# Performance work log

Measured on AMD Instinct MI355X. Metric: run time of the kernel, lower is better.

## Reference

```python
import jax, jax.numpy as jnp
import numpy as np

D_MODEL = 1024
NUM_HEADS = 16
D_K = D_MODEL // NUM_HEADS


def setup_inputs() -> dict:
    key = jax.random.key(0)
    ks = jax.random.split(key, 9)
    s = 1.0 / np.sqrt(D_MODEL)
    x = jax.random.normal(ks[0], (1, 4096, D_MODEL), dtype=jnp.float32)
    Wq = jax.random.uniform(ks[1], (D_MODEL, D_MODEL), jnp.float32, -s, s)
    bq = jax.random.uniform(ks[2], (D_MODEL,), jnp.float32, -s, s)
    Wk = jax.random.uniform(ks[3], (D_MODEL, D_MODEL), jnp.float32, -s, s)
    bk = jax.random.uniform(ks[4], (D_MODEL,), jnp.float32, -s, s)
    Wv = jax.random.uniform(ks[5], (D_MODEL, D_MODEL), jnp.float32, -s, s)
    bv = jax.random.uniform(ks[6], (D_MODEL,), jnp.float32, -s, s)
    Wo = jax.random.uniform(ks[7], (D_MODEL, D_MODEL), jnp.float32, -s, s)
    bo = jax.random.uniform(ks[8], (D_MODEL,), jnp.float32, -s, s)
    return {"x": x, "Wq": Wq, "bq": bq, "Wk": Wk, "bk": bk,
            "Wv": Wv, "bv": bv, "Wo": Wo, "bo": bo}


def reference(x, Wq, bq, Wk, bk, Wv, bv, Wo, bo):
    B, S, _ = x.shape
    scale = jnp.sqrt(jnp.asarray(D_K, dtype=x.dtype))
    # projections (torch Linear: y = x @ W.T + b)
    q = (x @ Wq.T + bq).reshape(B, S, NUM_HEADS, D_K).transpose(0, 2, 1, 3)
    k = (x @ Wk.T + bk).reshape(B, S, NUM_HEADS, D_K).transpose(0, 2, 1, 3)
    v = (x @ Wv.T + bv).reshape(B, S, NUM_HEADS, D_K).transpose(0, 2, 1, 3)
    # [B, H, S, S] naive scores, causal mask, softmax
    scores = jnp.einsum('bhqd,bhkd->bhqk', q, k) / scale
    causal = jnp.tril(jnp.ones((S, S), dtype=bool))
    scores = jnp.where(causal, scores, jnp.asarray(-jnp.inf, dtype=scores.dtype))
    probs = jax.nn.softmax(scores, axis=-1)
    out = jnp.einsum('bhqk,bhkd->bhqd', probs, v)
    out = out.transpose(0, 2, 1, 3).reshape(B, S, D_MODEL)
    return out @ Wo.T + bo
```

## Files before the change

### kernel.cpp

```cpp
#include <hip/hip_runtime.h>
#include <math.h>

#define SEQ 4096
#define DMODEL 1024
#define NH 16
#define DK 64
#define LDP 72

typedef __bf16    bf16x8 __attribute__((ext_vector_type(8)));
typedef float     f32x4  __attribute__((ext_vector_type(4)));
typedef __fp16    fp16x2 __attribute__((ext_vector_type(2)));
typedef _Float16  h16x2  __attribute__((ext_vector_type(2)));
typedef _Float16  h16x4  __attribute__((ext_vector_type(4)));
typedef _Float16  h16x8  __attribute__((ext_vector_type(8)));

#define GLOAD_LDS16(g, l) __builtin_amdgcn_global_load_lds(                     \
    (const __attribute__((address_space(1))) unsigned int*)(g),                 \
    (__attribute__((address_space(3))) unsigned int*)(l), 16, 0, 0)

__device__ __forceinline__ h16x2 cvt_pk_h16(float a, float b) {
    fp16x2 r = __builtin_amdgcn_cvt_pkrtz(a, b);
    return __builtin_bit_cast(h16x2, r);
}

#define EXP2R(x) __builtin_amdgcn_exp2f(x)

__global__ __launch_bounds__(256)
void cvt_all(const float* __restrict__ x, const float* __restrict__ Wq,
             const float* __restrict__ Wk, const float* __restrict__ Wv,
             const float* __restrict__ Wo, __bf16* __restrict__ dst)
{
    const size_t M1 = 1u << 20;
    const size_t e = ((size_t)blockIdx.x * 256 + threadIdx.x) * 8;
    const float* src; size_t off;
    if      (e < 4*M1) { src = x;  off = e;        }
    else if (e < 5*M1) { src = Wq; off = e - 4*M1; }
    else if (e < 6*M1) { src = Wk; off = e - 5*M1; }
    else if (e < 7*M1) { src = Wv; off = e - 6*M1; }
    else               { src = Wo; off = e - 7*M1; }
    const float4 f0 = *reinterpret_cast<const float4*>(&src[off]);
    const float4 f1 = *reinterpret_cast<const float4*>(&src[off + 4]);
    bf16x8 pk;
    pk[0]=(__bf16)f0.x; pk[1]=(__bf16)f0.y; pk[2]=(__bf16)f0.z; pk[3]=(__bf16)f0.w;
    pk[4]=(__bf16)f1.x; pk[5]=(__bf16)f1.y; pk[6]=(__bf16)f1.z; pk[7]=(__bf16)f1.w;
    *reinterpret_cast<bf16x8*>(&dst[e]) = pk;
}

__device__ __forceinline__ void gemm_core128(const __bf16* __restrict__ A,
                                             const __bf16* __restrict__ W,
                                             int m0, int n0, int t,
                                             __bf16* AsF, __bf16* BsF,
                                             f32x4 acc[4][4])
{
    const int w = t >> 6, lane = t & 63, l15 = lane & 15, quad = lane >> 4;
    const int wm = (w & 1) * 64, wn = (w >> 1) * 64;
    const int lr = lane >> 3, lc = lane & 7;
    for (int k0 = 0; k0 < DMODEL; k0 += 64) {
        __syncthreads();
        #pragma unroll
        for (int p = 0; p < 4; ++p) {
            const int n = w*4 + p;
            const int r = n*8 + lr;
            const int cl = lc ^ (r & 7);
            GLOAD_LDS16(&A[(size_t)(m0 + r) * DMODEL + k0 + cl*8], &AsF[n*512]);
            GLOAD_LDS16(&W[(size_t)(n0 + r) * DMODEL + k0 + cl*8], &BsF[n*512]);
        }
        __syncthreads();
        #pragma unroll
        for (int kb = 0; kb < 2; ++kb) {
            const int phys = ((kb*4 + quad) ^ (l15 & 7)) * 8;
            bf16x8 af[4], bfr[4];
            #pragma unroll
            for (int i = 0; i < 4; ++i) {
                af[i]  = *reinterpret_cast<const bf16x8*>(&AsF[(wm + i*16 + l15)*64 + phys]);
                bfr[i] = *reinterpret_cast<const bf16x8*>(&BsF[(wn + i*16 + l15)*64 + phys]);
            }
            #pragma unroll
            for (int ms = 0; ms < 4; ++ms)
                #pragma unroll
                for (int ns = 0; ns < 4; ++ns)
                    acc[ms][ns] = __builtin_amdgcn_mfma_f32_16x16x32_bf16(af[ms], bfr[ns], acc[ms][ns], 0, 0, 0);
        }
    }
}

__global__ __launch_bounds__(256, 3)
void gemm_qkv(const __bf16* __restrict__ xb, const __bf16* __restrict__ Wcat,
              const float* __restrict__ bq, const float* __restrict__ bk,
              const float* __restrict__ bv,
              _Float16* __restrict__ Qh, _Float16* __restrict__ Kh, _Float16* __restrict__ Vth)
{
    __shared__ __bf16 SM[4*64*LDP];
    __bf16* AsF = SM;
    __bf16* BsF = SM + 8192;
    const int t = threadIdx.x;
    const int n0g = blockIdx.x * 128;
    const int m0  = blockIdx.y * 128;
    const int which = n0g >> 10;
    const int n_in  = n0g & 1023;

    f32x4 acc[4][4] = {};
    gemm_core128(xb, Wcat, m0, n0g, t, AsF, BsF, acc);

    const int w = t >> 6, lane = t & 63, l15 = lane & 15, quad = lane >> 4;
    const int wm = (w & 1) * 64, wn = (w >> 1) * 64;
    const float* bias = (which == 0) ? bq : (which == 1) ? bk : bv;
    float br[4];
    #pragma unroll
    for (int ns = 0; ns < 4; ++ns) br[ns] = bias[n_in + wn + ns*16 + l15];

    if (which == 2) {
        #pragma unroll
        for (int ms = 0; ms < 4; ++ms)
            #pragma unroll
            for (int ns = 0; ns < 4; ++ns) {
                h16x4 pk;
                #pragma unroll
                for (int rg = 0; rg < 4; ++rg) pk[rg] = (_Float16)(acc[ms][ns][rg] + br[ns]);
                *reinterpret_cast<h16x4*>(
                    &Vth[(size_t)(n_in + wn + ns*16 + l15) * SEQ + m0 + wm + ms*16 + quad*4]) = pk;
            }
    } else {
        const float s = (which == 0) ? 0.1803368787f : 1.0f;
        _Float16* C = (which == 0) ? Qh : Kh;
        __syncthreads();
        _Float16* tile = (_Float16*)SM + w * 64 * LDP;
        #pragma unroll
        for (int ms = 0; ms < 4; ++ms)
            #pragma unroll
            for (int ns = 0; ns < 4; ++ns)
                #pragma unroll
                for (int rg = 0; rg < 4; ++rg)
                    tile[(ms*16 + quad*4 + rg) * LDP + ns*16 + l15] =
                        (_Float16)((acc[ms][ns][rg] + br[ns]) * s);
        asm volatile("s_waitcnt lgkmcnt(0)" ::: "memory");
        const int er = lane >> 3, ec = (lane & 7) * 8;
        #pragma unroll
        for (int p = 0; p < 8; ++p) {
            const h16x8 v = *reinterpret_cast<const h16x8*>(&tile[(er + p*8) * LDP + ec]);
            *reinterpret_cast<h16x8*>(
                &C[(size_t)(m0 + wm + er + p*8) * DMODEL + n_in + wn + ec]) = v;
        }
    }
}

__device__ __forceinline__ void gemm_core64(const __bf16* __restrict__ A,
                                            const __bf16* __restrict__ W,
                                            int m0, int n0, int t,
                                            __bf16* AsF, __bf16* BsF,
                                            f32x4 acc[2][4])
{
    const int w = t >> 6, lane = t & 63, l15 = lane & 15, quad = lane >> 4;
    const int lr = lane >> 3, lc = lane & 7;
    for (int k0 = 0; k0 < DMODEL; k0 += 64) {
        __syncthreads();
        #pragma unroll
        for (int p = 0; p < 4; ++p) {
            const int n = w*4 + p;
            const int r = n*8 + lr;
            const int cl = lc ^ (r & 7);
            GLOAD_LDS16(&A[(size_t)(m0 + r) * DMODEL + k0 + cl*8], &AsF[n*512]);
        }
        #pragma unroll
        for (int p = 0; p < 2; ++p) {
            const int n = w*2 + p;
            const int r = n*8 + lr;
            const int cl = lc ^ (r & 7);
            GLOAD_LDS16(&W[(size_t)(n0 + r) * DMODEL + k0 + cl*8], &BsF[n*512]);
        }
        __syncthreads();
        #pragma unroll
        for (int kb = 0; kb < 2; ++kb) {
            const int phys = ((kb*4 + quad) ^ (l15 & 7)) * 8;
            bf16x8 af0 = *reinterpret_cast<const bf16x8*>(&AsF[(w*32 + l15)*64 + phys]);
            bf16x8 af1 = *reinterpret_cast<const bf16x8*>(&AsF[(w*32 + 16 + l15)*64 + phys]);
            #pragma unroll
            for (int ns = 0; ns < 4; ++ns) {
                const bf16x8 bfr = *reinterpret_cast<const bf16x8*>(&BsF[(ns*16 + l15)*64 + phys]);
                acc[0][ns] = __builtin_amdgcn_mfma_f32_16x16x32_bf16(af0, bfr, acc[0][ns], 0, 0, 0);
                acc[1][ns] = __builtin_amdgcn_mfma_f32_16x16x32_bf16(af1, bfr, acc[1][ns], 0, 0, 0);
            }
        }
    }
}

__global__ __launch_bounds__(256, 4)
void gemm_out(const __bf16* __restrict__ Ob, const __bf16* __restrict__ Wob,
              const float* __restrict__ bo, float* __restrict__ out)
{
    __shared__ __bf16 AsF[128*64];
    __shared__ __bf16 BsF[64*64];
    const int t = threadIdx.x;
    const int n0 = blockIdx.x * 64;
    const int m0 = blockIdx.y * 128;

    f32x4 acc[2][4] = {};
    gemm_core64(Ob, Wob, m0, n0, t, AsF, BsF, acc);

    const int lane = t & 63, l15 = lane & 15, quad = lane >> 4, w = t >> 6;
    float br[4];
    #pragma unroll
    for (int ns = 0; ns < 4; ++ns) br[ns] = bo[n0 + ns*16 + l15];
    #pragma unroll
    for (int ms = 0; ms < 2; ++ms)
        #pragma unroll
        for (int ns = 0; ns < 4; ++ns)
            #pragma unroll
            for (int rg = 0; rg < 4; ++rg)
                out[(size_t)(m0 + w*32 + ms*16 + quad*4 + rg) * DMODEL + n0 + ns*16 + l15] =
                    acc[ms][ns][rg] + br[ns];
}

__global__ __launch_bounds__(256, 3)
void attn_mfma(const _Float16* __restrict__ Q, const _Float16* __restrict__ K,
               const _Float16* __restrict__ Vt, __bf16* __restrict__ O,
               _Float16* __restrict__ partA, _Float16* __restrict__ partB,
               float* __restrict__ lpart)
{
    __shared__ _Float16 KsF[2][64*64];
    __shared__ _Float16 VsF[2][64*64];

    const int t = threadIdx.x;
    const int w = t >> 6;
    const int lane = t & 63, l15 = lane & 15, quad = lane >> 4;
    const int lr = lane >> 3, lc = lane & 7;
    const int h = blockIdx.y;
    const int u = blockIdx.x;

    const int cl = lc ^ lr;
    const int rA = (w*2 + 0)*8 + lr, rB = (w*2 + 1)*8 + lr;
    const int dA = (w*2 + 0)*512,   dB = (w*2 + 1)*512;
    const h16x4 vone = {(_Float16)1.f, (_Float16)1.f, (_Float16)1.f, (_Float16)1.f};

    int g = u * 22;
    const int gend = g + 22;
    int qt = 0;
    while ((qt + 1) * (qt + 2) <= g) ++qt;

    while (g < gend) {
        const int S = qt * (qt + 1);
        const int rowlen = 2*qt + 2;
        const int ts = g - S;
        const int rem = gend - S;
        const int te = (rowlen < rem) ? rowlen : rem;
        const int s0 = qt*128 + w*16;
        const int s1 = s0 + 64;

        h16x8 bq8[2][2];
        #pragma unroll
        for (int kb = 0; kb < 2; ++kb) {
            bq8[0][kb] = *reinterpret_cast<const h16x8*>(
                &Q[(size_t)(s0 + l15) * DMODEL + h*DK + kb*32 + quad*8]);
            bq8[1][kb] = *reinterpret_cast<const h16x8*>(
                &Q[(size_t)(s1 + l15) * DMODEL + h*DK + kb*32 + quad*8]);
        }

        const _Float16* kpA = &K [(size_t)(ts*64 + rA) * DMODEL + h*DK + cl*8];
        const _Float16* kpB = &K [(size_t)(ts*64 + rB) * DMODEL + h*DK + cl*8];
        const _Float16* vpA = &Vt[(size_t)(h*DK + rA) * SEQ + ts*64 + cl*8];
        const _Float16* vpB = &Vt[(size_t)(h*DK + rB) * SEQ + ts*64 + cl*8];

#define STAGE_KV(bi) do {                                     \
        GLOAD_LDS16(kpA, &KsF[bi][dA]);                       \
        GLOAD_LDS16(kpB, &KsF[bi][dB]);                       \
        GLOAD_LDS16(vpA, &VsF[bi][dA]);                       \
        GLOAD_LDS16(vpB, &VsF[bi][dB]);                       \
        kpA += (size_t)64*DMODEL; kpB += (size_t)64*DMODEL;   \
        vpA += 64; vpB += 64; } while (0)

        f32x4 acc[2][4] = {};
        f32x4 accl[2] = {};

        STAGE_KV(0);
        __syncthreads();

        int pbuf = 0;
        for (int tk = ts; tk < te; ++tk, pbuf ^= 1) {
            if (tk + 1 < te) STAGE_KV(pbuf ^ 1);

            const int j0 = tk * 64;
            const bool act0 = (j0 <= s0 + 15);
            const bool msk0 = (j0 + 63 > s0);
            const bool msk1 = (j0 + 63 > s1);
            const int rel0 = s0 - j0 + l15;
            const int rel1 = s1 - j0 + l15;

            h16x4 ap[2][4];
            #pragma unroll
            for (int st = 0; st < 4; ++st) {
                const h16x8 ak0 = *reinterpret_cast<const h16x8*>(
                    &KsF[pbuf][(st*16 + l15)*64 + ((quad ^ (l15 & 7)))*8]);
                const h16x8 ak1 = *reinterpret_cast<const h16x8*>(
                    &KsF[pbuf][(st*16 + l15)*64 + (((4 + quad) ^ (l15 & 7)))*8]);
                {
                    f32x4 cc = {0.f, 0.f, 0.f, 0.f};
                    cc = __builtin_amdgcn_mfma_f32_16x16x32_f16(ak0, bq8[1][0], cc, 0, 0, 0);
                    cc = __builtin_amdgcn_mfma_f32_16x16x32_f16(ak1, bq8[1][1], cc, 0, 0, 0);
                    float pv[4];
                    if (msk1) {
                        #pragma unroll
                        for (int rg = 0; rg < 4; ++rg) {
                            const float e = EXP2R(cc[rg]);
                            pv[rg] = (st*16 + quad*4 + rg > rel1) ? 0.f : e;
                        }
                    } else {
                        #pragma unroll
                        for (int rg = 0; rg < 4; ++rg) pv[rg] = EXP2R(cc[rg]);
                    }
                    const h16x2 lo = cvt_pk_h16(pv[0], pv[1]);
                    const h16x2 hi = cvt_pk_h16(pv[2], pv[3]);
                    ap[1][st] = (h16x4){lo[0], lo[1], hi[0], hi[1]};
                    accl[1] = __builtin_amdgcn_mfma_f32_16x16x16f16(ap[1][st], vone, accl[1], 0, 0, 0);
                }
                if (act0) {
                    f32x4 cc = {0.f, 0.f, 0.f, 0.f};
                    cc = __builtin_amdgcn_mfma_f32_16x16x32_f16(ak0, bq8[0][0], cc, 0, 0, 0);
                    cc = __builtin_amdgcn_mfma_f32_16x16x32_f16(ak1, bq8[0][1], cc, 0, 0, 0);
                    float pv[4];
                    if (msk0) {
                        #pragma unroll
                        for (int rg = 0; rg < 4; ++rg) {
                            const float e = EXP2R(cc[rg]);
                            pv[rg] = (st*16 + quad*4 + rg > rel0) ? 0.f : e;
                        }
                    } else {
                        #pragma unroll
                        for (int rg = 0; rg < 4; ++rg) pv[rg] = EXP2R(cc[rg]);
                    }
                    const h16x2 lo = cvt_pk_h16(pv[0], pv[1]);
                    const h16x2 hi = cvt_pk_h16(pv[2], pv[3]);
                    ap[0][st] = (h16x4){lo[0], lo[1], hi[0], hi[1]};
                    accl[0] = __builtin_amdgcn_mfma_f32_16x16x16f16(ap[0][st], vone, accl[0], 0, 0, 0);
                }
            }

            #pragma unroll
            for (int ds_ = 0; ds_ < 4; ++ds_) {
                #pragma unroll
                for (int st = 0; st < 4; ++st) {
                    const h16x4 bv = *reinterpret_cast<const h16x4*>(
                        &VsF[pbuf][(ds_*16 + l15)*64 +
                                   (((st*2 + (quad >> 1)) ^ (l15 & 7)))*8 + (quad & 1)*4]);
                    acc[1][ds_] = __builtin_amdgcn_mfma_f32_16x16x16f16(ap[1][st], bv, acc[1][ds_], 0, 0, 0);
                    if (act0)
                        acc[0][ds_] = __builtin_amdgcn_mfma_f32_16x16x16f16(ap[0][st], bv, acc[0][ds_], 0, 0, 0);
                }
            }
            __syncthreads();
        }
#undef STAGE_KV

        if (ts == 0 && te == rowlen) {
            #pragma unroll
            for (int s = 0; s < 2; ++s) {
                const int base = s ? s1 : s0;
                #pragma unroll
                for (int rg = 0; rg < 4; ++rg) {
                    const float inv = 1.0f / accl[s][rg];
                    const size_t row = (size_t)(base + quad*4 + rg) * DMODEL + h * DK;
                    #pragma unroll
                    for (int ds_ = 0; ds_ < 4; ++ds_)
                        O[row + ds_*16 + l15] = (__bf16)(acc[s][ds_][rg] * inv);
                }
            }
        } else {
            const int side = (g == u*22) ? 0 : 1;
            const int slot = (h*48 + u)*2 + side;
            _Float16* p = (slot < 1024) ? partA + (size_t)slot * 8192
                                        : partB + (size_t)(slot - 1024) * 8192;
            #pragma unroll
            for (int s = 0; s < 2; ++s) {
                #pragma unroll
                for (int rg = 0; rg < 4; ++rg) {
                    const int lrow = s*64 + w*16 + quad*4 + rg;
                    #pragma unroll
                    for (int ds_ = 0; ds_ < 4; ++ds_)
                        p[lrow*64 + ds_*16 + l15] = (_Float16)acc[s][ds_][rg];
                    if (l15 == 0) lpart[(size_t)slot*128 + lrow] = accl[s][rg];
                }
            }
        }
        g = S + te;
        ++qt;
    }
}

__global__ __launch_bounds__(256)
void attn_combine(const _Float16* __restrict__ partA, const _Float16* __restrict__ partB,
                  const float* __restrict__ lpart, __bf16* __restrict__ O)
{
    const int t = threadIdx.x;
    const int qt = blockIdx.x;
    const int h  = blockIdx.y;
    const int S = qt*(qt+1);
    const int rowlen = 2*qt + 2;
    const int c0 = S / 22;
    const int c1 = (S + rowlen - 1) / 22;
    if (c0 == c1) return;
    const int r  = t >> 1;
    const int d0 = (t & 1) * 32;

    float a[4][8] = {};
    float l = 0.f;
    for (int c = c0; c <= c1; ++c) {
        const int side = (22*c >= S) ? 0 : 1;
        const int sl = (h*48 + c)*2 + side;
        const _Float16* pc = (sl < 1024) ? partA + (size_t)sl * 8192
                                         : partB + (size_t)(sl - 1024) * 8192;
        l += lpart[(size_t)sl*128 + r];
        #pragma unroll
        for (int i = 0; i < 4; ++i) {
            const h16x8 v = *reinterpret_cast<const h16x8*>(&pc[r*64 + d0 + i*8]);
            #pragma unroll
            for (int j = 0; j < 8; ++j) a[i][j] += (float)v[j];
        }
    }
    const float inv = 1.0f / l;
    const size_t grow = (size_t)(qt*128 + r) * DMODEL + h*64 + d0;
    #pragma unroll
    for (int i = 0; i < 4; ++i) {
        bf16x8 pk;
        #pragma unroll
        for (int j = 0; j < 8; ++j) pk[j] = (__bf16)(a[i][j] * inv);
        *reinterpret_cast<bf16x8*>(&O[grow + i*8]) = pk;
    }
}

extern "C" void kernel_launch(void* const* d_in, const int* in_sizes, int n_in,
                              void* d_out, int out_size, void* d_ws, size_t ws_size,
                              hipStream_t stream) {
    const float* x  = (const float*)d_in[0];
    const float* Wq = (const float*)d_in[1];
    const float* bq = (const float*)d_in[2];
    const float* Wk = (const float*)d_in[3];
    const float* bk = (const float*)d_in[4];
    const float* Wv = (const float*)d_in[5];
    const float* bv = (const float*)d_in[6];
    const float* Wo = (const float*)d_in[7];
    const float* bo = (const float*)d_in[8];
    float* out = (float*)d_out;

    const size_t M1 = 1u << 20;
    __bf16* base = (__bf16*)d_ws;
    __bf16*    xb   = base;
    __bf16*    Wcat = base + 4*M1;
    __bf16*    Wob  = base + 7*M1;
    _Float16*  Qh   = (_Float16*)(base + 8*M1);
    _Float16*  Kh   = (_Float16*)(base + 12*M1);
    _Float16*  Vth  = (_Float16*)(base + 16*M1);
    __bf16*    Ob   = base + 20*M1;
    _Float16*  partA = (_Float16*)out;
    _Float16*  partB = (_Float16*)xb;
    float*     lpart = (float*)Wcat;

    cvt_all<<<4096, 256, 0, stream>>>(x, Wq, Wk, Wv, Wo, base);
    gemm_qkv<<<dim3(24, 32), 256, 0, stream>>>(xb, Wcat, bq, bk, bv, Qh, Kh, Vth);
    attn_mfma<<<dim3(48, NH), 256, 0, stream>>>(Qh, Kh, Vth, Ob, partA, partB, lpart);
    attn_combine<<<dim3(32, NH), 256, 0, stream>>>(partA, partB, lpart, Ob);
    gemm_out<<<dim3(16, 32), 256, 0, stream>>>(Ob, Wob, bo, out);
}
```

Measured before the change: 206.7 us.

## Rebalance causal attention work split into 64 segments per head with compile-time slot map

Splits each head's 1056 causal tiles into 64 segments of 16-17 tiles instead of 48 segments of 22. This gives 1024 blocks, which matches 256 CUs at four blocks each, and the launch bound is raised from 3 to 4 blocks per SM. A constexpr map assigns compact partial-result slots and is used by both the attention and combine kernels. The grid is reordered so heads vary fastest, which changes block scheduling order. The risks are register pressure from the higher occupancy bound and the new placement of partial buffers in the workspace.

```diff
diff --git a/kernel.cpp b/kernel.cpp
--- a/kernel.cpp
+++ b/kernel.cpp
@@ -5,6 +5,7 @@
 #define DMODEL 1024
 #define NH 16
 #define DK 64
+#define NU 64
 #define LDP 72
 
 typedef __bf16    bf16x8 __attribute__((ext_vector_type(8)));
@@ -24,6 +25,48 @@
 }
 
 #define EXP2R(x) __builtin_amdgcn_exp2f(x)
+
+struct UMap {
+    short ustart[NU + 1];
+    short slotHead[NU];
+    short slotTail[NU];
+    short nslot;
+};
+constexpr UMap makeUMap() {
+    UMap m{};
+    int g = 0;
+    for (int u = 0; u < NU; ++u) {
+        m.ustart[u] = (short)g;
+        g += (((u >> 4) & 1) ? 16 : 17);
+    }
+    m.ustart[NU] = (short)g;
+    int slot = 0;
+    for (int u = 0; u < NU; ++u) {
+        m.slotHead[u] = -1; m.slotTail[u] = -1;
+        const int gs = m.ustart[u], ge = m.ustart[u + 1];
+        int gg = gs;
+        int qt = 0;
+        while ((qt + 1) * (qt + 2) <= gg) ++qt;
+        while (gg < ge) {
+            const int S = qt * (qt + 1), len = 2 * qt + 2;
+            const int ts = gg - S;
+            const int rem = ge - S;
+            const int te = (len < rem) ? len : rem;
+            const bool full = (ts == 0) && (te == len);
+            if (!full) {
+                if (gg == gs) m.slotHead[u] = (short)slot++;
+                else          m.slotTail[u] = (short)slot++;
+            }
+            gg = S + te;
+            ++qt;
+        }
+    }
+    m.nslot = (short)slot;
+    return m;
+}
+__device__ constexpr UMap UM = makeUMap();
+static_assert(makeUMap().ustart[NU] == 1056, "tile total");
+static_assert(makeUMap().nslot <= 116, "slot capacity: 16*nslot <= 1856");
 
 __global__ __launch_bounds__(256)
 void cvt_all(const float* __restrict__ x, const float* __restrict__ Wq,
@@ -211,7 +254,7 @@
                     acc[ms][ns][rg] + br[ns];
 }
 
-__global__ __launch_bounds__(256, 3)
+__global__ __launch_bounds__(256, 4)
 void attn_mfma(const _Float16* __restrict__ Q, const _Float16* __restrict__ K,
                const _Float16* __restrict__ Vt, __bf16* __restrict__ O,
                _Float16* __restrict__ partA, _Float16* __restrict__ partB,
@@ -224,16 +267,17 @@
     const int w = t >> 6;
     const int lane = t & 63, l15 = lane & 15, quad = lane >> 4;
     const int lr = lane >> 3, lc = lane & 7;
-    const int h = blockIdx.y;
-    const int u = blockIdx.x;
+    const int h = blockIdx.x;
+    const int u = blockIdx.y;
 
     const int cl = lc ^ lr;
     const int rA = (w*2 + 0)*8 + lr, rB = (w*2 + 1)*8 + lr;
     const int dA = (w*2 + 0)*512,   dB = (w*2 + 1)*512;
     const h16x4 vone = {(_Float16)1.f, (_Float16)1.f, (_Float16)1.f, (_Float16)1.f};
 
-    int g = u * 22;
-    const int gend = g + 22;
+    int g = UM.ustart[u];
+    const int gend = UM.ustart[u + 1];
+    const int gseg0 = g;
     int qt = 0;
     while ((qt + 1) * (qt + 2) <= g) ++qt;
 
@@ -364,8 +408,9 @@
                 }
             }
         } else {
-            const int side = (g == u*22) ? 0 : 1;
-            const int slot = (h*48 + u)*2 + side;
+            const bool isHead = (g == gseg0);
+            const int local = isHead ? UM.slotHead[u] : UM.slotTail[u];
+            const int slot = h * UM.nslot + local;
             _Float16* p = (slot < 1024) ? partA + (size_t)slot * 8192
                                         : partB + (size_t)(slot - 1024) * 8192;
             #pragma unroll
@@ -394,8 +439,8 @@
     const int h  = blockIdx.y;
     const int S = qt*(qt+1);
     const int rowlen = 2*qt + 2;
-    const int c0 = S / 22;
-    const int c1 = (S + rowlen - 1) / 22;
+    int c0 = 0; while (UM.ustart[c0+1] <= S) ++c0;
+    int c1 = c0; while (UM.ustart[c1+1] <= S + rowlen - 1) ++c1;
     if (c0 == c1) return;
     const int r  = t >> 1;
     const int d0 = (t & 1) * 32;
@@ -403,8 +448,10 @@
     float a[4][8] = {};
     float l = 0.f;
     for (int c = c0; c <= c1; ++c) {
-        const int side = (22*c >= S) ? 0 : 1;
-        const int sl = (h*48 + c)*2 + side;
+        const int local = (c == c0)
+            ? ((S == UM.ustart[c0]) ? UM.slotHead[c0] : UM.slotTail[c0])
+            : UM.slotHead[c];
+        const int sl = h * UM.nslot + local;
         const _Float16* pc = (sl < 1024) ? partA + (size_t)sl * 8192
                                          : partB + (size_t)(sl - 1024) * 8192;
         l += lpart[(size_t)sl*128 + r];
@@ -450,12 +497,12 @@
     _Float16*  Vth  = (_Float16*)(base + 16*M1);
     __bf16*    Ob   = base + 20*M1;
     _Float16*  partA = (_Float16*)out;
-    _Float16*  partB = (_Float16*)xb;
-    float*     lpart = (float*)Wcat;
+    _Float16*  partB = (_Float16*)d_ws;
+    float*     lpart = (float*)((char*)d_ws + 13*M1);
 
     cvt_all<<<4096, 256, 0, stream>>>(x, Wq, Wk, Wv, Wo, base);
     gemm_qkv<<<dim3(24, 32), 256, 0, stream>>>(xb, Wcat, bq, bk, bv, Qh, Kh, Vth);
-    attn_mfma<<<dim3(48, NH), 256, 0, stream>>>(Qh, Kh, Vth, Ob, partA, partB, lpart);
+    attn_mfma<<<dim3(NH, NU), 256, 0, stream>>>(Qh, Kh, Vth, Ob, partA, partB, lpart);
     attn_combine<<<dim3(32, NH), 256, 0, stream>>>(partA, partB, lpart, Ob);
     gemm_out<<<dim3(16, 32), 256, 0, stream>>>(Ob, Wob, bo, out);
 }
```

New measurement: 224.2 us. 1.08x slower.
